# Kernel optimization log

Hardware: AMD Instinct MI355X
Metric: run time of the kernel (lower is better)

The kernel has to match this reference:

```python
import jax, jax.numpy as jnp
import numpy as np
from jax import lax


def setup_inputs() -> dict:
    key = jax.random.key(0)
    k1, k2 = jax.random.split(key)
    B, N, D = 4, 4096, 128
    f_s = jax.random.normal(k1, (B, N, D), dtype=jnp.float32)
    f_trans = jax.random.normal(k2, (B, N, D), dtype=jnp.float32)
    return {"f_s": f_s, "f_trans": f_trans}


def reference(f_s, f_trans):
    temp = 10.0
    eps = 1e-8
    B, N, D = f_s.shape
    # pairwise dot products, reused for cosine sim and for the logits ("all")
    dots = jnp.einsum('bnd,bmd->bnm', f_s, f_trans)  # [B,N,M]
    norm_s = jnp.linalg.norm(f_s, axis=-1)       # [B,N]
    norm_t = jnp.linalg.norm(f_trans, axis=-1)   # [B,M]
    # torch.cosine_similarity: dot / max(|x|*|y|, eps)
    sim = dots / jnp.maximum(norm_s[:, :, None] * norm_t[:, None, :], eps)
    # argmax over dim=1 (the N axis) -> index per (b, m)
    idx = jnp.argmax(sim, axis=1)  # [B,M] int
    # gather f_trans rows at those indices (detached in the original via numpy)
    pos_q_trans = lax.stop_gradient(
        jnp.take_along_axis(f_trans, idx[..., None], axis=1))  # [B,M,D]
    pos_logit = jnp.sum(f_s * pos_q_trans, axis=-1) / temp  # [B,N] (N==M)
    pos_exp = jnp.exp(pos_logit)
    # sum_m exp(<f_s_n, f_trans_m>/temp) without materializing [B,N,M,D]
    all_exp = jnp.sum(jnp.exp(dots / temp), axis=-1)  # [B,N]
    ratio = jnp.clip(pos_exp / all_exp, 1e-40)
    loss = jnp.mean(jnp.sum(-jnp.log(ratio), axis=-1) / N)
    return loss
```

## Files before the change

### kernel.cpp

```cpp
#include <hip/hip_runtime.h>
#include <math.h>

#define BB 4
#define NN 4096
#define DD 128
#define HS 16
#define NIT 8
#define QG 32

typedef __attribute__((ext_vector_type(8))) short bf16x8;
typedef __attribute__((ext_vector_type(4))) float f32x4;
typedef __attribute__((ext_vector_type(4))) unsigned short u16x4;

__device__ __forceinline__ void mfma_16x16x32_bf16(f32x4& d, bf16x8 a, bf16x8 b) {
  asm volatile("v_mfma_f32_16x16x32_bf16 %0, %1, %2, %0" : "+v"(d) : "v"(a), "v"(b));
}

__device__ __forceinline__ void gload16(const void* g, void* lds) {
  __builtin_amdgcn_global_load_lds(
      (const __attribute__((address_space(1))) void*)g,
      (__attribute__((address_space(3))) void*)lds, 16, 0, 0);
}

__device__ __forceinline__ float vexp2(float x) {
  float r; asm("v_exp_f32 %0, %1" : "=v"(r) : "v"(x)); return r;
}

__device__ __forceinline__ unsigned short f2b(float x) {
  union { float f; unsigned u; } v; v.f = x;
  unsigned r = v.u + 0x7fffu + ((v.u >> 16) & 1u);
  return (unsigned short)(r >> 16);
}

__global__ __launch_bounds__(256) void k_prep(const float* __restrict__ fs,
                                              const float* __restrict__ ft,
                                              unsigned short* __restrict__ fsb,
                                              unsigned short* __restrict__ ftb,
                                              float* __restrict__ inv_norm) {
  int i = blockIdx.x * 256 + threadIdx.x;
  float4 a = ((const float4*)fs)[i];
  float4 c = ((const float4*)ft)[i];
  u16x4 oa; oa[0] = f2b(a.x); oa[1] = f2b(a.y); oa[2] = f2b(a.z); oa[3] = f2b(a.w);
  ((u16x4*)fsb)[i] = oa;
  const float C = 0.14426950408889634f;
  u16x4 oc; oc[0] = f2b(c.x * C); oc[1] = f2b(c.y * C);
  oc[2] = f2b(c.z * C); oc[3] = f2b(c.w * C);
  ((u16x4*)ftb)[i] = oc;
  float s = a.x * a.x + a.y * a.y + a.z * a.z + a.w * a.w;
#pragma unroll
  for (int off = 1; off <= 16; off <<= 1) s += __shfl_xor(s, off);
  if ((threadIdx.x & 31) == 0) inv_norm[i >> 5] = 1.0f / sqrtf(s);
}

__global__ __launch_bounds__(256, 6) void k_main(const unsigned short* __restrict__ fsb,
                                                 const unsigned short* __restrict__ ftb,
                                                 const float* __restrict__ inv_norm,
                                                 float* __restrict__ psum,
                                                 float2* __restrict__ pmax) {
  __shared__ __align__(16) char smem[20480];
  float* psb = (float*)(smem + 16384);

  const int t = threadIdx.x;
  const int w = t >> 6, lane = t & 63;
  const int l15 = lane & 15, g = lane >> 4;
  const int bid = blockIdx.x;
  const int q = bid & 31, h = (bid >> 5) & 15, b = bid >> 9;
  const int m0 = q * 128 + w * 32;

  const int r0 = t >> 4, cp0 = t & 15;
  const int src0 = r0 * 256 + ((cp0 ^ (r0 & 15)) << 4);
  const int src1 = (16 + r0) * 256 + ((cp0 ^ ((16 + r0) & 15)) << 4);
  const int lds0 = w * 1024, lds1 = 4096 + w * 1024;

  const unsigned short* Ab = ftb + ((size_t)b * NN + m0) * DD;
  bf16x8 af[4][2];
#pragma unroll
  for (int kk = 0; kk < 4; kk++)
#pragma unroll
    for (int mf = 0; mf < 2; mf++)
      af[kk][mf] = *(const bf16x8*)(Ab + (mf * 16 + l15) * DD + kk * 32 + g * 8);

  const char* gB0 = (const char*)(fsb + ((size_t)b * NN + h * 256) * DD);
  const float* invb = inv_norm + (size_t)b * NN + h * 256;

  char* cb = smem;
  char* nb = smem + 8192;

  gload16(gB0 + src0, cb + lds0);
  gload16(gB0 + src1, cb + lds1);

  float bkey[2][4];
#pragma unroll
  for (int mf = 0; mf < 2; mf++)
#pragma unroll
    for (int j = 0; j < 4; j++) bkey[mf][j] = 0.0f;

#pragma unroll 1
  for (int it = 0; it < NIT; ++it) {
    __syncthreads();
    if (it + 1 < NIT) {
      const char* gBn = gB0 + (it + 1) * 8192;
      gload16(gBn + src0, nb + lds0);
      gload16(gBn + src1, nb + lds1);
    }
    float svn[2];
#pragma unroll
    for (int fj = 0; fj < 2; fj++) svn[fj] = invb[it * 32 + fj * 16 + l15];

    f32x4 acc[2][2] = {};
#pragma unroll
    for (int kk = 0; kk < 4; kk++) {
      bf16x8 bf[2];
#pragma unroll
      for (int fj = 0; fj < 2; fj++)
        bf[fj] = *(const bf16x8*)(cb + (fj * 16 + l15) * 256 + (((kk * 4 + g) ^ l15) << 4));
#pragma unroll
      for (int mf = 0; mf < 2; mf++)
#pragma unroll
        for (int fj = 0; fj < 2; fj++)
          mfma_16x16x32_bf16(acc[mf][fj], af[kk][mf], bf[fj]);
    }
#pragma unroll
    for (int fj = 0; fj < 2; fj++) {
      float e0 = vexp2(acc[0][fj][0]), e1 = vexp2(acc[0][fj][1]);
      float e2 = vexp2(acc[0][fj][2]), e3 = vexp2(acc[0][fj][3]);
      float e4 = vexp2(acc[1][fj][0]), e5 = vexp2(acc[1][fj][1]);
      float e6 = vexp2(acc[1][fj][2]), e7 = vexp2(acc[1][fj][3]);
      float s = ((e0 + e1) + (e2 + e3)) + ((e4 + e5) + (e6 + e7));
      s += __shfl_xor(s, 16);
      s += __shfl_xor(s, 32);
      if (g == 0) psb[w * 256 + it * 32 + fj * 16 + l15] = s;
    }
    const unsigned codebase = (unsigned)((7 - it) << 1);
#pragma unroll
    for (int fj = 0; fj < 2; fj++) {
      const unsigned code = codebase | (unsigned)(1 - fj);
#pragma unroll
      for (int mf = 0; mf < 2; mf++)
#pragma unroll
        for (int j = 0; j < 4; j++) {
          float v = fmaf(acc[mf][fj][j], svn[fj], 4.0f);
          unsigned kb = (__float_as_uint(v) & 0xFFFFFFF0u) | code;
          bkey[mf][j] = fmaxf(bkey[mf][j], __uint_as_float(kb));
        }
    }
    char* tmp = cb; cb = nb; nb = tmp;
  }
  __syncthreads();

  {
    float s4 = (psb[t] + psb[256 + t]) + (psb[512 + t] + psb[768 + t]);
    psum[((size_t)(b * QG + q)) * NN + h * 256 + t] = s4;
  }

#pragma unroll
  for (int mf = 0; mf < 2; mf++)
#pragma unroll
    for (int j = 0; j < 4; j++) {
      unsigned bits = __float_as_uint(bkey[mf][j]);
      unsigned code = bits & 15u;
      int itw = 7 - (int)(code >> 1);
      int fjw = 1 - (int)(code & 1u);
      int n = h * 256 + itw * 32 + fjw * 16 + l15;
      float vq = __uint_as_float(bits & 0xFFFFFFF0u);
#pragma unroll
      for (int off = 1; off <= 8; off <<= 1) {
        float ov = __shfl_xor(vq, off);
        int   on = __shfl_xor(n, off);
        if (ov > vq || (ov == vq && on < n)) { vq = ov; n = on; }
      }
      if (l15 == 0) {
        int m = m0 + mf * 16 + g * 4 + j;
        float2 pr; pr.x = vq; pr.y = __int_as_float(n);
        pmax[((size_t)b * NN + m) * HS + h] = pr;
      }
    }
}

__global__ __launch_bounds__(256) void k_post(const float* __restrict__ fs,
                                              const float* __restrict__ ft,
                                              const float* __restrict__ psum,
                                              const float2* __restrict__ pmax,
                                              float* __restrict__ blockpart) {
  __shared__ float part[4];
  int w = threadIdx.x >> 6, lane = threadIdx.x & 63;
  int row = blockIdx.x * 4 + w;
  int b = row >> 12, pn = row & (NN - 1);
  float v = -INFINITY; int i = 0x7fffffff;
  if (lane < HS) {
    float2 pm = pmax[(size_t)row * HS + lane];
    v = pm.x; i = __float_as_int(pm.y);
  }
#pragma unroll
  for (int off = 1; off <= 8; off <<= 1) {
    float ov = __shfl_xor(v, off);
    int   oi = __shfl_xor(i, off);
    if (ov > v || (ov == v && oi < i)) { v = ov; i = oi; }
  }
  int j = __shfl(i, 0);
  float tot = (lane < QG) ? psum[((size_t)(b * QG + lane)) * NN + pn] : 0.0f;
#pragma unroll
  for (int off = 1; off <= 16; off <<= 1) tot += __shfl_xor(tot, off);
  float2 a = ((const float2*)(fs + (size_t)row * DD))[lane];
  float2 c = ((const float2*)(ft + ((size_t)b * NN + j) * DD))[lane];
  float s = a.x * c.x + a.y * c.y;
#pragma unroll
  for (int off = 32; off > 0; off >>= 1) s += __shfl_xor(s, off);
  if (lane == 0) {
    float term = logf(tot) - s * 0.1f;
    part[w] = fminf(term, 92.103403719761827f);
  }
  __syncthreads();
  if (threadIdx.x == 0)
    blockpart[blockIdx.x] = part[0] + part[1] + part[2] + part[3];
}

__global__ __launch_bounds__(256) void k_final(const float* __restrict__ blockpart,
                                               float* __restrict__ out) {
  __shared__ float red[256];
  float s = 0.0f;
  for (int i = threadIdx.x; i < (BB * NN) / 4; i += 256) s += blockpart[i];
  red[threadIdx.x] = s;
  __syncthreads();
  for (int st = 128; st > 0; st >>= 1) {
    if (threadIdx.x < st) red[threadIdx.x] += red[threadIdx.x + st];
    __syncthreads();
  }
  if (threadIdx.x == 0) out[0] = red[0] * (1.0f / (BB * NN));
}

extern "C" void kernel_launch(void* const* d_in, const int* in_sizes, int n_in,
                              void* d_out, int out_size, void* d_ws, size_t ws_size,
                              hipStream_t stream) {
  const float* fs = (const float*)d_in[0];
  const float* ft = (const float*)d_in[1];
  float* out = (float*)d_out;

  const size_t NE = (size_t)BB * NN * DD;
  unsigned short* fsb = (unsigned short*)d_ws;
  unsigned short* ftb = fsb + NE;
  float*  inv_norm = (float*)(ftb + NE);
  float*  psum     = inv_norm + (size_t)BB * NN;
  float2* pmax     = (float2*)(psum + (size_t)BB * QG * NN);
  float*  blockpart = (float*)(pmax + (size_t)BB * NN * HS);

  k_prep<<<(int)(NE / 4 / 256), 256, 0, stream>>>(fs, ft, fsb, ftb, inv_norm);
  k_main<<<BB * HS * QG, 256, 0, stream>>>(fsb, ftb, inv_norm, psum, pmax);
  k_post<<<(BB * NN) / 4, 256, 0, stream>>>(fs, ft, psum, pmax, blockpart);
  k_final<<<1, 256, 0, stream>>>(blockpart, out);
}
```

Baseline: 64.77 us.

## Triple-buffer B tiles with vmcnt-gated barriers and stage inverse norms in LDS

Replaces the double-buffered LDS pipeline with a three-buffer ring that prefetches two tiles ahead. Each iteration waits with s_waitcnt vmcnt(2) before a raw s_barrier instead of a full __syncthreads, so more global loads stay in flight. The inverse norms for the block are also loaded once into LDS rather than read from global memory each iteration, and the last iteration is peeled. In exchange, LDS grows and launch bounds drop from 6 to 5 blocks per CU, which lowers occupancy.

After: 55.91 us. 1.16x faster.

```diff
diff --git a/kernel.cpp b/kernel.cpp
--- a/kernel.cpp
+++ b/kernel.cpp
@@ -52,13 +52,14 @@
   if ((threadIdx.x & 31) == 0) inv_norm[i >> 5] = 1.0f / sqrtf(s);
 }
 
-__global__ __launch_bounds__(256, 6) void k_main(const unsigned short* __restrict__ fsb,
+__global__ __launch_bounds__(256, 5) void k_main(const unsigned short* __restrict__ fsb,
                                                  const unsigned short* __restrict__ ftb,
                                                  const float* __restrict__ inv_norm,
                                                  float* __restrict__ psum,
                                                  float2* __restrict__ pmax) {
-  __shared__ __align__(16) char smem[20480];
-  float* psb = (float*)(smem + 16384);
+  __shared__ __align__(16) char smem[29696];
+  float* psb  = (float*)(smem + 24576);
+  float* sInv = (float*)(smem + 28672);
 
   const int t = threadIdx.x;
   const int w = t >> 6, lane = t & 63;
@@ -80,14 +81,20 @@
     for (int mf = 0; mf < 2; mf++)
       af[kk][mf] = *(const bf16x8*)(Ab + (mf * 16 + l15) * DD + kk * 32 + g * 8);
 
+  sInv[t] = inv_norm[(size_t)b * NN + h * 256 + t];
+
   const char* gB0 = (const char*)(fsb + ((size_t)b * NN + h * 256) * DD);
-  const float* invb = inv_norm + (size_t)b * NN + h * 256;
-
-  char* cb = smem;
-  char* nb = smem + 8192;
-
-  gload16(gB0 + src0, cb + lds0);
-  gload16(gB0 + src1, cb + lds1);
+
+  __syncthreads();
+
+  char* b0 = smem;
+  char* b1 = smem + 8192;
+  char* b2 = smem + 16384;
+
+  gload16(gB0 + src0, b0 + lds0);
+  gload16(gB0 + src1, b0 + lds1);
+  gload16(gB0 + 8192 + src0, b1 + lds0);
+  gload16(gB0 + 8192 + src1, b1 + lds1);
 
   float bkey[2][4];
 #pragma unroll
@@ -96,16 +103,17 @@
     for (int j = 0; j < 4; j++) bkey[mf][j] = 0.0f;
 
 #pragma unroll 1
-  for (int it = 0; it < NIT; ++it) {
-    __syncthreads();
-    if (it + 1 < NIT) {
-      const char* gBn = gB0 + (it + 1) * 8192;
-      gload16(gBn + src0, nb + lds0);
-      gload16(gBn + src1, nb + lds1);
+  for (int it = 0; it < NIT - 1; ++it) {
+    asm volatile("s_waitcnt vmcnt(2)" ::: "memory");
+    __builtin_amdgcn_s_barrier();
+    if (it < NIT - 2) {
+      const char* gBn = gB0 + (it + 2) * 8192;
+      gload16(gBn + src0, b2 + lds0);
+      gload16(gBn + src1, b2 + lds1);
     }
     float svn[2];
-#pragma unroll
-    for (int fj = 0; fj < 2; fj++) svn[fj] = invb[it * 32 + fj * 16 + l15];
+    svn[0] = sInv[it * 32 + l15];
+    svn[1] = sInv[it * 32 + 16 + l15];
 
     f32x4 acc[2][2] = {};
 #pragma unroll
@@ -113,7 +121,7 @@
       bf16x8 bf[2];
 #pragma unroll
       for (int fj = 0; fj < 2; fj++)
-        bf[fj] = *(const bf16x8*)(cb + (fj * 16 + l15) * 256 + (((kk * 4 + g) ^ l15) << 4));
+        bf[fj] = *(const bf16x8*)(b0 + (fj * 16 + l15) * 256 + (((kk * 4 + g) ^ l15) << 4));
 #pragma unroll
       for (int mf = 0; mf < 2; mf++)
 #pragma unroll
@@ -144,7 +152,53 @@
           bkey[mf][j] = fmaxf(bkey[mf][j], __uint_as_float(kb));
         }
     }
-    char* tmp = cb; cb = nb; nb = tmp;
+    char* tmp = b0; b0 = b1; b1 = b2; b2 = tmp;
+  }
+
+  {
+    const int it = NIT - 1;
+    asm volatile("s_waitcnt vmcnt(0)" ::: "memory");
+    __builtin_amdgcn_s_barrier();
+    float svn[2];
+    svn[0] = sInv[it * 32 + l15];
+    svn[1] = sInv[it * 32 + 16 + l15];
+    f32x4 acc[2][2] = {};
+#pragma unroll
+    for (int kk = 0; kk < 4; kk++) {
+      bf16x8 bf[2];
+#pragma unroll
+      for (int fj = 0; fj < 2; fj++)
+        bf[fj] = *(const bf16x8*)(b0 + (fj * 16 + l15) * 256 + (((kk * 4 + g) ^ l15) << 4));
+#pragma unroll
+      for (int mf = 0; mf < 2; mf++)
+#pragma unroll
+        for (int fj = 0; fj < 2; fj++)
+          mfma_16x16x32_bf16(acc[mf][fj], af[kk][mf], bf[fj]);
+    }
+#pragma unroll
+    for (int fj = 0; fj < 2; fj++) {
+      float e0 = vexp2(acc[0][fj][0]), e1 = vexp2(acc[0][fj][1]);
+      float e2 = vexp2(acc[0][fj][2]), e3 = vexp2(acc[0][fj][3]);
+      float e4 = vexp2(acc[1][fj][0]), e5 = vexp2(acc[1][fj][1]);
+      float e6 = vexp2(acc[1][fj][2]), e7 = vexp2(acc[1][fj][3]);
+      float s = ((e0 + e1) + (e2 + e3)) + ((e4 + e5) + (e6 + e7));
+      s += __shfl_xor(s, 16);
+      s += __shfl_xor(s, 32);
+      if (g == 0) psb[w * 256 + it * 32 + fj * 16 + l15] = s;
+    }
+    const unsigned codebase = 0u;
+#pragma unroll
+    for (int fj = 0; fj < 2; fj++) {
+      const unsigned code = codebase | (unsigned)(1 - fj);
+#pragma unroll
+      for (int mf = 0; mf < 2; mf++)
+#pragma unroll
+        for (int j = 0; j < 4; j++) {
+          float v = fmaf(acc[mf][fj][j], svn[fj], 4.0f);
+          unsigned kb = (__float_as_uint(v) & 0xFFFFFFF0u) | code;
+          bkey[mf][j] = fmaxf(bkey[mf][j], __uint_as_float(kb));
+        }
+    }
   }
   __syncthreads();
 
```

## Enlarge k_main tiles and stream B fragments via registers instead of LDS

Applied to the files above, without the earlier changes.

Each k_main block now covers 256 m-rows and 512 n-columns, up from 128 and 256. Each wave holds 4 A fragments instead of 2. The B tiles are loaded straight from global memory into registers, double-buffered in software, which removes the LDS staging and the per-iteration __syncthreads. This cuts grid size and the psum/pmax partial outputs, so k_post is adjusted to match, and the argmax key now needs 5 low bits to encode 16 iterations. The risks are higher register pressure (occupancy hint drops from 6 to 2), uncoalesced-ish direct global fragment loads, and slightly coarser key precision.

New measurement: 64.76 us. No clear change (-0.0%).

```diff
diff --git a/kernel.cpp b/kernel.cpp
--- a/kernel.cpp
+++ b/kernel.cpp
@@ -4,9 +4,9 @@
 #define BB 4
 #define NN 4096
 #define DD 128
-#define HS 16
-#define NIT 8
-#define QG 32
+#define HS 8
+#define NT2 16
+#define QG 16
 
 typedef __attribute__((ext_vector_type(8))) short bf16x8;
 typedef __attribute__((ext_vector_type(4))) float f32x4;
@@ -14,12 +14,6 @@
 
 __device__ __forceinline__ void mfma_16x16x32_bf16(f32x4& d, bf16x8 a, bf16x8 b) {
   asm volatile("v_mfma_f32_16x16x32_bf16 %0, %1, %2, %0" : "+v"(d) : "v"(a), "v"(b));
-}
-
-__device__ __forceinline__ void gload16(const void* g, void* lds) {
-  __builtin_amdgcn_global_load_lds(
-      (const __attribute__((address_space(1))) void*)g,
-      (__attribute__((address_space(3))) void*)lds, 16, 0, 0);
 }
 
 __device__ __forceinline__ float vexp2(float x) {
@@ -52,117 +46,109 @@
   if ((threadIdx.x & 31) == 0) inv_norm[i >> 5] = 1.0f / sqrtf(s);
 }
 
-__global__ __launch_bounds__(256, 6) void k_main(const unsigned short* __restrict__ fsb,
+__global__ __launch_bounds__(256, 2) void k_main(const unsigned short* __restrict__ fsb,
                                                  const unsigned short* __restrict__ ftb,
                                                  const float* __restrict__ inv_norm,
                                                  float* __restrict__ psum,
                                                  float2* __restrict__ pmax) {
-  __shared__ __align__(16) char smem[20480];
-  float* psb = (float*)(smem + 16384);
+  __shared__ float psb[4 * 512];
+  __shared__ float sInv[512];
 
   const int t = threadIdx.x;
   const int w = t >> 6, lane = t & 63;
   const int l15 = lane & 15, g = lane >> 4;
   const int bid = blockIdx.x;
-  const int q = bid & 31, h = (bid >> 5) & 15, b = bid >> 9;
-  const int m0 = q * 128 + w * 32;
-
-  const int r0 = t >> 4, cp0 = t & 15;
-  const int src0 = r0 * 256 + ((cp0 ^ (r0 & 15)) << 4);
-  const int src1 = (16 + r0) * 256 + ((cp0 ^ ((16 + r0) & 15)) << 4);
-  const int lds0 = w * 1024, lds1 = 4096 + w * 1024;
+  const int qg = bid & 15, h = (bid >> 4) & 7, b = bid >> 7;
+  const int m0 = qg * 256 + w * 64;
 
   const unsigned short* Ab = ftb + ((size_t)b * NN + m0) * DD;
-  bf16x8 af[4][2];
+  bf16x8 af[4][4];
 #pragma unroll
   for (int kk = 0; kk < 4; kk++)
 #pragma unroll
-    for (int mf = 0; mf < 2; mf++)
+    for (int mf = 0; mf < 4; mf++)
       af[kk][mf] = *(const bf16x8*)(Ab + (mf * 16 + l15) * DD + kk * 32 + g * 8);
 
-  const char* gB0 = (const char*)(fsb + ((size_t)b * NN + h * 256) * DD);
-  const float* invb = inv_norm + (size_t)b * NN + h * 256;
-
-  char* cb = smem;
-  char* nb = smem + 8192;
-
-  gload16(gB0 + src0, cb + lds0);
-  gload16(gB0 + src1, cb + lds1);
-
-  float bkey[2][4];
-#pragma unroll
-  for (int mf = 0; mf < 2; mf++)
+  sInv[t] = inv_norm[(size_t)b * NN + h * 512 + t];
+  sInv[256 + t] = inv_norm[(size_t)b * NN + h * 512 + 256 + t];
+  __syncthreads();
+
+  const char* gBlane = (const char*)(fsb + ((size_t)b * NN + h * 512) * DD)
+                       + l15 * 256 + g * 16;
+
+  float bkey[4][4];
+#pragma unroll
+  for (int mf = 0; mf < 4; mf++)
 #pragma unroll
     for (int j = 0; j < 4; j++) bkey[mf][j] = 0.0f;
 
+  bf16x8 bfA[8], bfB[8];
+
+#define LOAD_TILE(dst, it)                                                   \
+  {                                                                          \
+    const char* p = gBlane + (it) * 8192;                                    \
+    _Pragma("unroll")                                                        \
+    for (int kk = 0; kk < 4; kk++) {                                         \
+      dst[kk * 2 + 0] = *(const bf16x8*)(p + kk * 64);                       \
+      dst[kk * 2 + 1] = *(const bf16x8*)(p + 4096 + kk * 64);                \
+    }                                                                        \
+  }
+
+#define COMPUTE_TILE(bf, it)                                                 \
+  {                                                                          \
+    f32x4 acc[4][2] = {};                                                    \
+    _Pragma("unroll")                                                        \
+    for (int kk = 0; kk < 4; kk++)                                           \
+      _Pragma("unroll")                                                      \
+      for (int mf = 0; mf < 4; mf++) {                                       \
+        mfma_16x16x32_bf16(acc[mf][0], af[kk][mf], bf[kk * 2 + 0]);          \
+        mfma_16x16x32_bf16(acc[mf][1], af[kk][mf], bf[kk * 2 + 1]);          \
+      }                                                                      \
+    _Pragma("unroll")                                                        \
+    for (int fj = 0; fj < 2; fj++) {                                         \
+      float s = 0.0f;                                                        \
+      _Pragma("unroll")                                                      \
+      for (int mf = 0; mf < 4; mf++) {                                       \
+        float e0 = vexp2(acc[mf][fj][0]), e1 = vexp2(acc[mf][fj][1]);        \
+        float e2 = vexp2(acc[mf][fj][2]), e3 = vexp2(acc[mf][fj][3]);        \
+        s += (e0 + e1) + (e2 + e3);                                          \
+      }                                                                      \
+      s += __shfl_xor(s, 16);                                                \
+      s += __shfl_xor(s, 32);                                                \
+      if (g == 0) psb[w * 512 + (it) * 32 + fj * 16 + l15] = s;              \
+      float svn = sInv[(it) * 32 + fj * 16 + l15];                           \
+      const unsigned code = (unsigned)((15 - (it)) << 1) | (unsigned)(1 - fj);\
+      _Pragma("unroll")                                                      \
+      for (int mf = 0; mf < 4; mf++)                                         \
+        _Pragma("unroll")                                                    \
+        for (int j = 0; j < 4; j++) {                                        \
+          float v = fmaf(acc[mf][fj][j], svn, 4.0f);                         \
+          unsigned kb = (__float_as_uint(v) & 0xFFFFFFE0u) | code;           \
+          bkey[mf][j] = fmaxf(bkey[mf][j], __uint_as_float(kb));             \
+        }                                                                    \
+    }                                                                        \
+  }
+
+  LOAD_TILE(bfA, 0)
 #pragma unroll 1
-  for (int it = 0; it < NIT; ++it) {
-    __syncthreads();
-    if (it + 1 < NIT) {
-      const char* gBn = gB0 + (it + 1) * 8192;
-      gload16(gBn + src0, nb + lds0);
-      gload16(gBn + src1, nb + lds1);
-    }
-    float svn[2];
-#pragma unroll
-    for (int fj = 0; fj < 2; fj++) svn[fj] = invb[it * 32 + fj * 16 + l15];
-
-    f32x4 acc[2][2] = {};
-#pragma unroll
-    for (int kk = 0; kk < 4; kk++) {
-      bf16x8 bf[2];
-#pragma unroll
-      for (int fj = 0; fj < 2; fj++)
-        bf[fj] = *(const bf16x8*)(cb + (fj * 16 + l15) * 256 + (((kk * 4 + g) ^ l15) << 4));
-#pragma unroll
-      for (int mf = 0; mf < 2; mf++)
-#pragma unroll
-        for (int fj = 0; fj < 2; fj++)
-          mfma_16x16x32_bf16(acc[mf][fj], af[kk][mf], bf[fj]);
-    }
-#pragma unroll
-    for (int fj = 0; fj < 2; fj++) {
-      float e0 = vexp2(acc[0][fj][0]), e1 = vexp2(acc[0][fj][1]);
-      float e2 = vexp2(acc[0][fj][2]), e3 = vexp2(acc[0][fj][3]);
-      float e4 = vexp2(acc[1][fj][0]), e5 = vexp2(acc[1][fj][1]);
-      float e6 = vexp2(acc[1][fj][2]), e7 = vexp2(acc[1][fj][3]);
-      float s = ((e0 + e1) + (e2 + e3)) + ((e4 + e5) + (e6 + e7));
-      s += __shfl_xor(s, 16);
-      s += __shfl_xor(s, 32);
-      if (g == 0) psb[w * 256 + it * 32 + fj * 16 + l15] = s;
-    }
-    const unsigned codebase = (unsigned)((7 - it) << 1);
-#pragma unroll
-    for (int fj = 0; fj < 2; fj++) {
-      const unsigned code = codebase | (unsigned)(1 - fj);
-#pragma unroll
-      for (int mf = 0; mf < 2; mf++)
-#pragma unroll
-        for (int j = 0; j < 4; j++) {
-          float v = fmaf(acc[mf][fj][j], svn[fj], 4.0f);
-          unsigned kb = (__float_as_uint(v) & 0xFFFFFFF0u) | code;
-          bkey[mf][j] = fmaxf(bkey[mf][j], __uint_as_float(kb));
-        }
-    }
-    char* tmp = cb; cb = nb; nb = tmp;
-  }
-  __syncthreads();
-
-  {
-    float s4 = (psb[t] + psb[256 + t]) + (psb[512 + t] + psb[768 + t]);
-    psum[((size_t)(b * QG + q)) * NN + h * 256 + t] = s4;
-  }
-
-#pragma unroll
-  for (int mf = 0; mf < 2; mf++)
+  for (int itp = 0; itp < NT2 / 2; ++itp) {
+    const int it0 = itp * 2, it1 = itp * 2 + 1;
+    LOAD_TILE(bfB, it1)
+    COMPUTE_TILE(bfA, it0)
+    if (itp < NT2 / 2 - 1) LOAD_TILE(bfA, it1 + 1)
+    COMPUTE_TILE(bfB, it1)
+  }
+
+#pragma unroll
+  for (int mf = 0; mf < 4; mf++)
 #pragma unroll
     for (int j = 0; j < 4; j++) {
       unsigned bits = __float_as_uint(bkey[mf][j]);
-      unsigned code = bits & 15u;
-      int itw = 7 - (int)(code >> 1);
+      unsigned code = bits & 31u;
+      int itw = 15 - (int)(code >> 1);
       int fjw = 1 - (int)(code & 1u);
-      int n = h * 256 + itw * 32 + fjw * 16 + l15;
-      float vq = __uint_as_float(bits & 0xFFFFFFF0u);
+      int n = h * 512 + itw * 32 + fjw * 16 + l15;
+      float vq = __uint_as_float(bits & 0xFFFFFFE0u);
 #pragma unroll
       for (int off = 1; off <= 8; off <<= 1) {
         float ov = __shfl_xor(vq, off);
@@ -175,6 +161,17 @@
         pmax[((size_t)b * NN + m) * HS + h] = pr;
       }
     }
+
+  __syncthreads();
+
+#pragma unroll
+  for (int rr = 0; rr < 2; rr++) {
+    int nl = rr * 256 + t;
+    float s4 = (psb[nl] + psb[512 + nl]) + (psb[1024 + nl] + psb[1536 + nl]);
+    psum[((size_t)(b * QG + qg)) * NN + h * 512 + nl] = s4;
+  }
+#undef LOAD_TILE
+#undef COMPUTE_TILE
 }
 
 __global__ __launch_bounds__(256) void k_post(const float* __restrict__ fs,
@@ -192,7 +189,7 @@
     v = pm.x; i = __float_as_int(pm.y);
   }
 #pragma unroll
-  for (int off = 1; off <= 8; off <<= 1) {
+  for (int off = 1; off <= 4; off <<= 1) {
     float ov = __shfl_xor(v, off);
     int   oi = __shfl_xor(i, off);
     if (ov > v || (ov == v && oi < i)) { v = ov; i = oi; }
@@ -200,7 +197,7 @@
   int j = __shfl(i, 0);
   float tot = (lane < QG) ? psum[((size_t)(b * QG + lane)) * NN + pn] : 0.0f;
 #pragma unroll
-  for (int off = 1; off <= 16; off <<= 1) tot += __shfl_xor(tot, off);
+  for (int off = 1; off <= 8; off <<= 1) tot += __shfl_xor(tot, off);
   float2 a = ((const float2*)(fs + (size_t)row * DD))[lane];
   float2 c = ((const float2*)(ft + ((size_t)b * NN + j) * DD))[lane];
   float s = a.x * c.x + a.y * c.y;
```
